# Performance work log

Hardware: AMD Instinct MI355X
Metric: run time of the kernel (lower is better)

## Reference

```python
import jax, jax.numpy as jnp
import numpy as np

B, N, F, S = 32, 512, 101, 10   # batch, set size, str_fea_len, expansion_size
E, H, L = 128, 4, 3             # embed_dim, num_heads, n_encoders
EH = E * H
TAB = 100                       # atom-feature table rows


def _ln(x, g, b, eps=1e-5):
    m = jnp.mean(x, -1, keepdims=True)
    v = jnp.var(x, -1, keepdims=True)
    return (x - m) / jnp.sqrt(v + eps) * g + b


def setup_inputs() -> dict:
    key = jax.random.key(0)
    ks = iter(jax.random.split(key, 48))
    nrm = lambda shape: jax.random.normal(next(ks), shape, jnp.float32) * 0.05
    return {
        'str_fea': jax.random.uniform(next(ks), (B, N, F), jnp.float32),
        'comp_fea': jax.random.randint(next(ks), (B, N), 0, TAB),
        'cell_fea': jax.random.normal(next(ks), (B, 6), jnp.float32),
        'af_table': jax.random.uniform(next(ks), (TAB, 92), jnp.float32),
        'comp_w': nrm((92, E)), 'comp_b': jnp.zeros((E,), jnp.float32),
        'emb_w': nrm(((F - 1) * S, E)), 'emb_b': jnp.zeros((E,), jnp.float32),
        'ln_g': jnp.ones((L, E), jnp.float32), 'ln_b': jnp.zeros((L, E), jnp.float32),
        'wq': nrm((L, E, EH)), 'bq': jnp.zeros((L, EH), jnp.float32),
        'wk': nrm((L, E, EH)), 'bk': jnp.zeros((L, EH), jnp.float32),
        'wv': nrm((L, E, EH)), 'bv': jnp.zeros((L, EH), jnp.float32),
        'inproj_w': nrm((L, EH, 3 * EH)), 'inproj_b': jnp.zeros((L, 3 * EH), jnp.float32),
        'out_w': nrm((L, EH, E)), 'out_b': jnp.zeros((L, E), jnp.float32),
        'ffn_w': nrm((L, E, E)), 'ffn_b': jnp.zeros((L, E), jnp.float32),
        'ln2_g': jnp.ones((E,), jnp.float32), 'ln2_b': jnp.zeros((E,), jnp.float32),
        'final_w': nrm((E, 1)), 'final_b': jnp.zeros((1,), jnp.float32),
    }


def reference(str_fea, comp_fea, cell_fea, af_table, comp_w, comp_b, emb_w, emb_b,
              ln_g, ln_b, wq, bq, wk, bk, wv, bv, inproj_w, inproj_b,
              out_w, out_b, ffn_w, ffn_b, ln2_g, ln2_b, final_w, final_b):
    weights = str_fea[:, :, 0:1]                                  # [B,N,1]
    # AtomFeaturizer + composition embedding
    comp = af_table[comp_fea] @ comp_w + comp_b                   # [B,N,E]
    # DistanceExpansion: (1 - (d - i/S))**2 for i in 0..S-1
    d = str_fea[:, :, 1:]                                         # [B,N,F-1]
    starter = jnp.arange(S, dtype=str_fea.dtype) / S
    de = (1.0 - (d[..., None] - starter)) ** 2                    # [B,N,F-1,S]
    de = de.reshape(d.shape[0], d.shape[1], (F - 1) * S)
    strf = de @ emb_w + emb_b                                     # [B,N,E]
    x = comp + strf
    x_init = x
    mask = jnp.sum(weights, -1) == 0.0                            # [B,N] key padding
    w_row = weights[..., 0]                                       # [B,N]
    hd = EH // H
    scale = 1.0 / np.sqrt(hd)
    for l in range(L):
        xn = _ln(x, ln_g[l], ln_b[l])
        qin = xn @ wq[l] + bq[l]                                  # [B,N,EH]
        kin = xn @ wk[l] + bk[l]
        vin = xn @ wv[l] + bv[l]                                  # used as V in manual attention
        # torch.nn.MultiheadAttention in-projection (v-block unused: att_output discarded)
        q = qin @ inproj_w[l][:, :EH] + inproj_b[l][:EH]
        k = kin @ inproj_w[l][:, EH:2 * EH] + inproj_b[l][EH:2 * EH]
        qh = q.reshape(q.shape[0], q.shape[1], H, hd)
        kh = k.reshape(k.shape[0], k.shape[1], H, hd)
        logits = jnp.einsum('bihd,bjhd->bhij', qh, kh) * scale    # [B,H,N,N]
        logits = jnp.where(mask[:, None, None, :], -1e9, logits)
        attn = jnp.mean(jax.nn.softmax(logits, -1), axis=1)       # head-averaged [B,N,N]
        # external edge-weight masking + renormalization
        aw = attn * w_row[:, None, :]
        aw = aw / jnp.sum(aw, -1, keepdims=True)
        att_out = jnp.einsum('bij,bjd->bid', aw, vin)             # [B,N,EH]
        o1 = x + att_out @ out_w[l] + out_b[l]
        o2 = jax.nn.softplus(_ln(o1, ln_g[l], ln_b[l]) @ ffn_w[l] + ffn_b[l])
        x = _ln(o1 + o2, ln_g[l], ln_b[l])
    x = jnp.sum(weights * (x + x_init), axis=1)                   # weighted pool [B,E]
    x = _ln(x, ln2_g, ln2_b)
    return x @ final_w + final_b                                  # [B,1]
```

## Files before the change

kernel.cpp:

```cpp
#include <hip/hip_runtime.h>
#include <math.h>

#define B_ 32
#define N_ 512
#define F_ 101
#define E_ 128
#define H_ 4
#define EH_ 512
#define L_ 3
#define M_ (B_*N_)

typedef __attribute__((ext_vector_type(8))) short s8v;
typedef __attribute__((ext_vector_type(8))) unsigned short us8v;
typedef __attribute__((ext_vector_type(4))) float f4v;
typedef __attribute__((ext_vector_type(4))) unsigned int u4v;

__device__ __forceinline__ unsigned short f2bf(float f){
  unsigned int u = __builtin_bit_cast(unsigned int, f);
  u += 0x7fffu + ((u>>16)&1u);
  return (unsigned short)(u>>16);
}
__device__ __forceinline__ float bf2f(unsigned int h){
  unsigned int u = h<<16; return __builtin_bit_cast(float, u);
}
__device__ __forceinline__ float softplus_f(float v) {
  return fmaxf(v, 0.f) + log1pf(__expf(-fabsf(v)));
}

#define GLOAD16(gp, lp) __builtin_amdgcn_global_load_lds( \
    (__attribute__((address_space(1))) unsigned int*)(gp), \
    (__attribute__((address_space(3))) unsigned int*)(lp), 16, 0, 0)

#define MFMA16(a,b,c) __builtin_amdgcn_mfma_f32_16x16x32_bf16(a,b,c,0,0,0)

__global__ __launch_bounds__(256) void prepA_kernel(
    const float* __restrict__ wq, const float* __restrict__ wk,
    const float* __restrict__ bq, const float* __restrict__ bk,
    const float* __restrict__ inproj_w,
    float* __restrict__ effpart, float* __restrict__ bpart) {
  __shared__ float As[64][132];
  __shared__ float Bs[64][68];
  const int blk = blockIdx.x;
  const int t = threadIdx.x;
  if (blk < 384) {
    const int bx = blk % 48, ks = blk / 48;
    const int lq = bx>>3, nt = bx&7;
    const int l = lq>>1, qk = lq&1;
    const int bn = nt*64;
    const int k0 = ks*64;
    const float* A = (qk ? wk : wq) + (size_t)l*128*512;
    const float* IP = inproj_w + (size_t)l*512*1536 + qk*512 + bn;
    float acc[8][4];
    #pragma unroll
    for (int i=0;i<8;++i)
      #pragma unroll
      for (int j=0;j<4;++j) acc[i][j]=0.f;
    const int r0 = (t&15)*8, c0 = (t>>4)*4;
    {
      int r = t & 127, half = t>>7;
      #pragma unroll
      for (int u=0;u<8;++u){
        float4 a = *(const float4*)(A + (size_t)r*512 + k0 + half*32 + u*4);
        int kk = half*32 + u*4;
        As[kk+0][r]=a.x; As[kk+1][r]=a.y; As[kk+2][r]=a.z; As[kk+3][r]=a.w;
      }
      int kk = t>>2, cb = (t&3)*16;
      #pragma unroll
      for (int u=0;u<4;++u)
        *(float4*)&Bs[kk][cb+u*4] = *(const float4*)(IP + (size_t)(k0+kk)*1536 + cb + u*4);
    }
    __syncthreads();
    for (int k2=0;k2<64;++k2){
      float4 b = *(const float4*)&Bs[k2][c0];
      float4 a0 = *(const float4*)&As[k2][r0];
      float4 a1 = *(const float4*)&As[k2][r0+4];
      float av[8] = {a0.x,a0.y,a0.z,a0.w,a1.x,a1.y,a1.z,a1.w};
      #pragma unroll
      for (int i=0;i<8;++i){
        acc[i][0] += av[i]*b.x; acc[i][1] += av[i]*b.y;
        acc[i][2] += av[i]*b.z; acc[i][3] += av[i]*b.w;
      }
    }
    #pragma unroll
    for (int j=0;j<4;++j){
      float* dst = effpart + (((size_t)ks*48 + bx)*64 + c0 + j)*128 + r0;
      float4 v0 = {acc[0][j], acc[1][j], acc[2][j], acc[3][j]};
      float4 v1 = {acc[4][j], acc[5][j], acc[6][j], acc[7][j]};
      *(float4*)dst = v0;
      *(float4*)(dst+4) = v1;
    }
  } else {
    const int idxb = blk - 384;
    const int lq = idxb>>3, kt = idxb&7;
    const int l = lq>>1, qk = lq&1;
    const float* bv = (qk?bk:bq) + l*512 + kt*64;
    const float* IP = inproj_w + ((size_t)l*512 + kt*64)*1536 + qk*512;
    float a0=0.f, a1=0.f;
    for (int kk=0; kk<64; ++kk){
      float b = bv[kk];
      const float* row = IP + (size_t)kk*1536;
      a0 += b*row[t];
      a1 += b*row[t+256];
    }
    bpart[(lq*8+kt)*512 + t]       = a0;
    bpart[(lq*8+kt)*512 + t + 256] = a1;
  }
}

__global__ __launch_bounds__(256) void prepB_kernel(
    const float* __restrict__ effpart, const float* __restrict__ bpart,
    const float* __restrict__ wv, const float* __restrict__ out_w,
    const float* __restrict__ ffn_w,
    const float* __restrict__ inproj_b, const float* __restrict__ bvv,
    const float* __restrict__ emb_w, const float* __restrict__ comp_w,
    const float* __restrict__ str_fea, const int* __restrict__ comp_fea,
    const float* __restrict__ af_table,
    unsigned short* __restrict__ wqkvT, unsigned short* __restrict__ outT,
    unsigned short* __restrict__ ffnT, float* __restrict__ bqkv,
    unsigned short* __restrict__ WHi, unsigned short* __restrict__ WLo,
    float* __restrict__ Cpart,
    unsigned short* __restrict__ FHi, unsigned short* __restrict__ FLo,
    float* __restrict__ w_row) {
  const int blk = blockIdx.x;
  const int t = threadIdx.x;
  if (blk < 1536) {
    int idx = blk*256 + t;
    int m = idx & 127;
    int n = (idx>>7) & 511;
    int lq = idx >> 16;
    int l = lq>>1, qk = lq&1;
    size_t base = (((size_t)(lq*8 + (n>>6)))*64 + (n&63))*128 + m;
    float v = 0.f;
    #pragma unroll
    for (int ks=0;ks<8;++ks) v += effpart[(size_t)ks*393216 + base];
    wqkvT[((size_t)l*1536 + qk*512 + n)*128 + m] = f2bf(v);
  } else if (blk < 1662) {
    const int b2 = blk - 1536;
    if (b2 < 108) {
      __shared__ float tile[64][65];
      const float* src; unsigned short* dst; int srcld, dstld;
      if (b2 < 48) {
        int lay = b2/16, rem = b2%16, kt = rem>>3, nt = rem&7;
        src = wv + ((size_t)lay*128 + kt*64)*512 + nt*64; srcld = 512;
        dst = wqkvT + ((size_t)lay*1536 + 1024 + nt*64)*128 + kt*64; dstld = 128;
      } else if (b2 < 96) {
        int b3 = b2-48; int lay = b3/16, rem = b3%16, kt = rem>>1, nt = rem&1;
        src = out_w + ((size_t)lay*512 + kt*64)*128 + nt*64; srcld = 128;
        dst = outT + ((size_t)lay*128 + nt*64)*512 + kt*64; dstld = 512;
      } else {
        int b4 = b2-96; int lay = b4/4, rem = b4%4, kt = rem>>1, nt = rem&1;
        src = ffn_w + ((size_t)lay*128 + kt*64)*128 + nt*64; srcld = 128;
        dst = ffnT + ((size_t)lay*128 + nt*64)*128 + kt*64; dstld = 128;
      }
      #pragma unroll
      for (int rp=0; rp<4; ++rp){
        int r = rp*16 + (t>>4), c = (t&15)*4;
        float4 v = *(const float4*)(src + (size_t)r*srcld + c);
        tile[r][c+0]=v.x; tile[r][c+1]=v.y; tile[r][c+2]=v.z; tile[r][c+3]=v.w;
      }
      __syncthreads();
      #pragma unroll
      for (int wp=0; wp<2; ++wp){
        int n = wp*32 + (t>>3), kk = (t&7)*8;
        us8v pk;
        #pragma unroll
        for (int e=0;e<8;++e) pk[e] = f2bf(tile[kk+e][n]);
        *(us8v*)(dst + (size_t)n*dstld + kk) = pk;
      }
    } else {
      int idx = (b2-108)*256 + t;
      if (idx < 4608) {
        int l = idx/1536, n = idx - l*1536;
        float v;
        if (n < 1024) {
          int qk = n>>9, c = n&511;
          v = inproj_b[(size_t)l*1536 + n];
          #pragma unroll
          for (int kt=0;kt<8;++kt) v += bpart[((l*2+qk)*8+kt)*512 + c];
        } else {
          v = bvv[(size_t)l*512 + (n-1024)];
        }
        bqkv[idx] = v;
      }
    }
  } else if (blk < 1674) {
    if (t < 128) {
      int p = blk - 1662, e = t;
      if (p < 10) {
        float Cp = 0.f;
        for (int ff=0; ff<10; ++ff){
          int f = p*10+ff;
          float A=0.f, Bv=0.f;
          #pragma unroll
          for (int s=0;s<10;++s){
            float wvv = emb_w[(size_t)(f*10+s)*128 + e];
            A += wvv; Bv += 0.2f*s*wvv; Cp += 0.01f*(s*s)*wvv;
          }
          int kA = 92+f, kB = 192+f;
          unsigned short hA = f2bf(A);
          WHi[e*320+kA]=hA; WLo[e*320+kA]=f2bf(A - bf2f(hA));
          unsigned short hB = f2bf(Bv);
          WHi[e*320+kB]=hB; WLo[e*320+kB]=f2bf(Bv - bf2f(hB));
        }
        Cpart[p*128+e] = Cp;
      } else if (p == 10) {
        for (int kk=0;kk<92;++kk){
          float v = comp_w[(size_t)kk*128 + e];
          unsigned short h = f2bf(v);
          WHi[e*320+kk]=h; WLo[e*320+kk]=f2bf(v - bf2f(h));
        }
      } else {
        for (int kk=292;kk<320;++kk){ WHi[e*320+kk]=0; WLo[e*320+kk]=0; }
      }
    }
  } else {
    int g = (blk-1674)*256 + t;
    int row = g / 40, seg = g - row*40;
    const float* sr = str_fea + (size_t)row*F_;
    if (seg == 0) w_row[row] = sr[0];
    const float* af = af_table + (size_t)comp_fea[row]*92;
    const int c0 = seg*8;
    us8v hi, lo;
    #pragma unroll
    for (int e=0;e<8;++e){
      int kk = c0+e; float v;
      if (kk < 92) v = af[kk];
      else if (kk < 192) { float u = 1.f - sr[1+kk-92]; v = u*u; }
      else if (kk < 292) v = 1.f - sr[1+kk-192];
      else v = 0.f;
      unsigned short h = f2bf(v);
      hi[e] = h; lo[e] = f2bf(v - bf2f(h));
    }
    *(us8v*)(FHi + (size_t)row*320 + c0) = hi;
    *(us8v*)(FLo + (size_t)row*320 + c0) = lo;
  }
}

__global__ __launch_bounds__(256) void embgemm_kernel(
    const unsigned short* __restrict__ FHi, const unsigned short* __restrict__ FLo,
    const unsigned short* __restrict__ WHi, const unsigned short* __restrict__ WLo,
    const float* __restrict__ Cpart, const float* __restrict__ comp_b,
    const float* __restrict__ emb_b,
    const float* __restrict__ g0, const float* __restrict__ b0,
    float* __restrict__ x, float* __restrict__ x_init,
    unsigned short* __restrict__ xnb) {
  __shared__ unsigned short lds[24576];
  unsigned short* AHi = lds;
  unsigned short* ALo = lds + 4096;
  unsigned short* BHi = lds + 8192;
  unsigned short* BLo = lds + 16384;
  const int bm = blockIdx.x*64;
  const int t = threadIdx.x, w = t>>6, l = t&63;
  f4v acc[8];
  #pragma unroll
  for (int i=0;i<8;++i) acc[i] = (f4v){0.f,0.f,0.f,0.f};
  const int srow = t>>3, sseg = t&7;
  for (int k0=0;k0<320;k0+=64){
    #pragma unroll
    for (int c=0;c<2;++c){
      int row = c*32+srow;
      GLOAD16(FHi + (size_t)(bm+row)*320 + k0 + ((sseg^(row&7))<<3), (char*)AHi + c*4096 + w*1024);
      GLOAD16(FLo + (size_t)(bm+row)*320 + k0 + ((sseg^(row&7))<<3), (char*)ALo + c*4096 + w*1024);
    }
    #pragma unroll
    for (int c=0;c<4;++c){
      int row = c*32+srow;
      GLOAD16(WHi + (size_t)row*320 + k0 + ((sseg^(row&7))<<3), (char*)BHi + c*4096 + w*1024);
      GLOAD16(WLo + (size_t)row*320 + k0 + ((sseg^(row&7))<<3), (char*)BLo + c*4096 + w*1024);
    }
    __syncthreads();
    #pragma unroll
    for (int ks=0;ks<2;++ks){
      int arow = w*16 + (l&15);
      int aswz = ((((l>>4)+ks*4) ^ (arow&7))<<4);
      s8v ah = *(const s8v*)((const char*)AHi + arow*128 + aswz);
      s8v al = *(const s8v*)((const char*)ALo + arow*128 + aswz);
      #pragma unroll
      for (int ct=0;ct<8;++ct){
        int col = ct*16 + (l&15);
        int bswz = ((((l>>4)+ks*4) ^ (col&7))<<4);
        s8v bh = *(const s8v*)((const char*)BHi + col*128 + bswz);
        s8v bl = *(const s8v*)((const char*)BLo + col*128 + bswz);
        acc[ct] = MFMA16(ah, bh, acc[ct]);
        acc[ct] = MFMA16(ah, bl, acc[ct]);
        acc[ct] = MFMA16(al, bh, acc[ct]);
      }
    }
    __syncthreads();
  }
  float vv[8][4], gc[8], bc[8];
  #pragma unroll
  for (int ct=0;ct<8;++ct){
    int c = ct*16 + (l&15);
    float be = comp_b[c] + emb_b[c];
    for (int p=0;p<10;++p) be += Cpart[p*128+c];
    gc[ct] = g0[c]; bc[ct] = b0[c];
    #pragma unroll
    for (int r=0;r<4;++r) vv[ct][r] = acc[ct][r] + be;
  }
  #pragma unroll
  for (int r=0;r<4;++r){
    float s=0.f, sq=0.f;
    #pragma unroll
    for (int ct=0;ct<8;++ct){ s += vv[ct][r]; sq += vv[ct][r]*vv[ct][r]; }
    #pragma unroll
    for (int m=1;m<16;m<<=1){ s += __shfl_xor(s,m,64); sq += __shfl_xor(sq,m,64); }
    float mean = s*(1.f/128.f);
    float rstd = rsqrtf(sq*(1.f/128.f) - mean*mean + 1e-5f);
    int row = bm + w*16 + (l>>4)*4 + r;
    #pragma unroll
    for (int ct=0;ct<8;++ct){
      int c = ct*16 + (l&15);
      float v = vv[ct][r];
      x[(size_t)row*128 + c] = v;
      x_init[(size_t)row*128 + c] = v;
      xnb[(size_t)row*128 + c] = f2bf((v-mean)*rstd*gc[ct] + bc[ct]);
    }
  }
}

template<int RT>
__global__ __launch_bounds__(256) void mgemm_kernel(
    const unsigned short* __restrict__ A,
    const unsigned short* __restrict__ Bt,
    const float* __restrict__ bias,
    unsigned short* __restrict__ Cb,
    unsigned short* __restrict__ vT,
    int K) {
  constexpr int BM = RT*32;
  __shared__ float smem[8192];
  unsigned short* Al = (unsigned short*)smem;
  unsigned short* Bl = Al + BM*64;
  const int bm = blockIdx.x*BM;
  const int bn = blockIdx.y*128;
  const int t = threadIdx.x;
  const int w = t>>6, l = t&63;
  const int wr = w>>1, wc = w&1;
  f4v acc[RT][4];
  #pragma unroll
  for (int i=0;i<RT;++i)
    #pragma unroll
    for (int j=0;j<4;++j) acc[i][j] = (f4v){0.f,0.f,0.f,0.f};
  const int srow = t>>3, sseg = t&7;
  for (int k0 = 0; k0 < K; k0 += 64) {
    #pragma unroll
    for (int c=0;c<BM/32;++c){
      int row = c*32 + srow;
      GLOAD16(A + (size_t)(bm+row)*K + k0 + ((sseg ^ (row&7))<<3),
              (char*)Al + c*4096 + w*1024);
    }
    #pragma unroll
    for (int c=0;c<4;++c){
      int row = c*32 + srow;
      GLOAD16(Bt + (size_t)(bn+row)*K + k0 + ((sseg ^ (row&7))<<3),
              (char*)Bl + c*4096 + w*1024);
    }
    __syncthreads();
    #pragma unroll
    for (int ks=0;ks<2;++ks){
      s8v bf[4];
      #pragma unroll
      for (int ct=0;ct<4;++ct){
        int col = wc*64 + ct*16 + (l&15);
        bf[ct] = *(const s8v*)((const char*)Bl + col*128 + ((((l>>4)+ks*4) ^ (col&7))<<4));
      }
      #pragma unroll
      for (int rt=0;rt<RT;++rt){
        int arow = wr*(RT*16) + rt*16 + (l&15);
        s8v af = *(const s8v*)((const char*)Al + arow*128 + ((((l>>4)+ks*4) ^ (arow&7))<<4));
        #pragma unroll
        for (int ct=0;ct<4;++ct)
          acc[rt][ct] = MFMA16(af, bf[ct], acc[rt][ct]);
      }
    }
    __syncthreads();
  }
  float bia[4];
  #pragma unroll
  for (int ct=0;ct<4;++ct) bia[ct] = bias[bn + wc*64 + ct*16 + (l&15)];
  unsigned short* lds16 = (unsigned short*)smem;
  if (bn < 1024) {
    #pragma unroll
    for (int rt=0;rt<RT;++rt)
      #pragma unroll
      for (int ct=0;ct<4;++ct)
        #pragma unroll
        for (int r=0;r<4;++r){
          int rr = wr*(RT*16) + rt*16 + (l>>4)*4 + r;
          int cc = wc*64 + ct*16 + (l&15);
          lds16[rr*128 + cc] = f2bf(acc[rt][ct][r] + bia[ct]);
        }
    __syncthreads();
    #pragma unroll
    for (int it=0; it<BM/16; ++it){
      int row = it*16 + (t>>4), seg = t&15;
      u4v v = *(const u4v*)(lds16 + row*128 + seg*8);
      *(u4v*)(Cb + (size_t)(bm+row)*1024 + bn + seg*8) = v;
    }
  } else {
    #pragma unroll
    for (int rt=0;rt<RT;++rt)
      #pragma unroll
      for (int ct=0;ct<4;++ct){
        int rbase = bm + wr*(RT*16) + rt*16 + (l>>4)*4;
        int bb = rbase >> 9, nn = rbase & 511;
        int d = bn - 1024 + wc*64 + ct*16 + (l&15);
        unsigned int lo = (unsigned int)f2bf(acc[rt][ct][0] + bia[ct])
                        | ((unsigned int)f2bf(acc[rt][ct][1] + bia[ct])<<16);
        unsigned int hi = (unsigned int)f2bf(acc[rt][ct][2] + bia[ct])
                        | ((unsigned int)f2bf(acc[rt][ct][3] + bia[ct])<<16);
        uint2 pk; pk.x = lo; pk.y = hi;
        *(uint2*)(vT + ((size_t)(bb*512 + d))*512 + nn) = pk;
      }
  }
}

#define STG_K5(dst, j0s) { \
  _Pragma("unroll") \
  for (int c_=0;c_<8;++c_){ \
    int row_ = c_*8 + w; \
    GLOAD16(qkb + (size_t)(b*512 + (j0s) + row_)*1024 + 512 + ((l ^ (row_&7))<<3), \
            (dst) + row_*1024); } }

#define STG_V5(j0s) { \
  _Pragma("unroll") \
  for (int c_=0;c_<8;++c_){ \
    int dbase_ = (c_*8 + w)*8; \
    GLOAD16(vT + ((size_t)(b*512 + dbase_ + (l>>3)))*512 + (j0s) + (((l&7) ^ (l>>3))<<3), \
            Vl + dbase_*128); } }

#define STG_B1(dst, k0s) { \
  _Pragma("unroll") \
  for (int c_=0;c_<2;++c_){ \
    int n_ = c_*64 + w*8 + (l>>3); \
    GLOAD16(outTl + (size_t)n_*512 + (k0s) + (((l&7) ^ (n_&7))<<3), \
            (dst) + (c_*64 + w*8)*128); } }

#define STG_F1() { \
  _Pragma("unroll") \
  for (int c2_=0;c2_<4;++c2_){ \
    int kh_ = c2_>>1, c_ = c2_&1; \
    int n_ = c_*64 + w*8 + (l>>3); \
    GLOAD16(ffnTl + (size_t)n_*128 + kh_*64 + (((l&7) ^ (n_&7))<<3), \
            ffnB + kh_*16384 + (c_*64 + w*8)*128); } }

__global__ __launch_bounds__(512, 2) void attnT_kernel(
    const unsigned short* __restrict__ qkb, const unsigned short* __restrict__ vT,
    const float* __restrict__ w_row,
    const unsigned short* __restrict__ outTl, const float* __restrict__ out_b,
    const unsigned short* __restrict__ ffnTl, const float* __restrict__ ffn_b,
    float* __restrict__ x, unsigned short* __restrict__ xnb,
    const float* __restrict__ g1, const float* __restrict__ b1,
    const float* __restrict__ g2, const float* __restrict__ b2) {
  __shared__ char smem[148736];
  char* const KbA = smem;
  char* const KbB = smem + 65536;
  char* const cA  = smem + 131072;
  float* const w_s    = (float*)(smem + 140288);
  float* const Spart  = (float*)(smem + 142336);
  float* const Rpart  = (float*)(smem + 144384);
  float* const sinv_l = (float*)(smem + 146432);
  float* const rho_l  = (float*)(smem + 147456);
  float* const zinv_l = (float*)(smem + 148480);
  char* const Vl = KbB;
  unsigned short* const outL = (unsigned short*)smem;
  char* const BtA = smem + 81920;
  char* const BtB = smem + 98304;
  float* const vst = (float*)(smem + 114688);
  char* const xnl  = smem;
  char* const ffnB = smem + 16384;

  const int id = blockIdx.x;
  const int b  = (id & 7) | ((id >> 6) << 3);
  const int i0 = ((id >> 3) & 7) * 64;
  const int bm = b*512 + i0;
  const int t = threadIdx.x, w = t>>6, l = t&63;
  const int wi = w & 3, wd = w >> 2;
  const float SC2 = 1.4426950408889634f * 0.088388347648318447f;

  for (int j=t; j<512; j+=512) w_s[j] = w_row[b*512+j];

  s8v qf[4][4];
  {
    const unsigned short* qbase = qkb + ((size_t)(b*512 + i0 + wi*16 + (l&15)))*1024;
    #pragma unroll
    for (int h=0;h<4;++h)
      #pragma unroll
      for (int ks=0;ks<4;++ks)
        qf[h][ks] = *(const s8v*)(qbase + h*128 + ks*32 + (l>>4)*8);
  }

  float sp[4][4], rp[4][4];
  #pragma unroll
  for (int h=0;h<4;++h)
    #pragma unroll
    for (int r=0;r<4;++r){ sp[h][r]=0.f; rp[h][r]=0.f; }

  STG_K5(KbA, 0);
  __syncthreads();

  {
    char* Kc = KbA; char* Kn = KbB;
    #pragma unroll 1
    for (int tt=0; tt<8; ++tt){
      if (tt < 7) STG_K5(Kn, (tt+1)*64);
      #pragma unroll
      for (int jsub=0;jsub<2;++jsub){
        const int jcol = wd*32 + jsub*16 + (l&15);
        const float wv = w_s[tt*64 + jcol];
        const float mw = (wv != 0.f) ? 1.f : 0.f;
        #pragma unroll
        for (int h=0;h<4;++h){
          f4v a = (f4v){0.f,0.f,0.f,0.f};
          #pragma unroll
          for (int ks=0;ks<4;++ks){
            int g = h*16 + ks*4 + (l>>4);
            s8v kf = *(const s8v*)(Kc + jcol*1024 + ((g ^ (jcol&7))<<4));
            a = MFMA16(qf[h][ks], kf, a);
          }
          #pragma unroll
          for (int r=0;r<4;++r){
            float e = exp2f(a[r]*SC2);
            sp[h][r] += e*mw;
            rp[h][r] += e*wv;
          }
        }
      }
      __syncthreads();
      char* tmp = Kc; Kc = Kn; Kn = tmp;
    }
  }

  #pragma unroll
  for (int h=0;h<4;++h)
    #pragma unroll
    for (int r=0;r<4;++r){
      float s = sp[h][r], rv = rp[h][r];
      s += __shfl_xor(s,1,64); rv += __shfl_xor(rv,1,64);
      s += __shfl_xor(s,2,64); rv += __shfl_xor(rv,2,64);
      s += __shfl_xor(s,4,64); rv += __shfl_xor(rv,4,64);
      s += __shfl_xor(s,8,64); rv += __shfl_xor(rv,8,64);
      sp[h][r] = s; rp[h][r] = rv;
    }
  if ((l&15)==0){
    int i = wi*16 + (l>>4)*4;
    #pragma unroll
    for (int h=0;h<4;++h)
      #pragma unroll
      for (int r=0;r<4;++r){
        Spart[(wd*4+h)*64 + i + r] = sp[h][r];
        Rpart[(wd*4+h)*64 + i + r] = rp[h][r];
      }
  }
  STG_K5(KbA, 0);
  STG_V5(0);
  __syncthreads();
  if (t < 256){
    int h = t>>6, i = t&63;
    float S = Spart[h*64+i] + Spart[(4+h)*64+i];
    float R = Rpart[h*64+i] + Rpart[(4+h)*64+i];
    float si = 1.f/S;
    sinv_l[h*64+i] = si;
    rho_l[h*64+i]  = R*si;
  }
  __syncthreads();
  if (t < 64)
    zinv_l[t] = 1.f/(rho_l[t] + rho_l[64+t] + rho_l[128+t] + rho_l[192+t]);
  __syncthreads();

  float siv[4][4], zv[4];
  {
    int ib = wi*16 + (l>>4)*4;
    #pragma unroll
    for (int h=0;h<4;++h)
      #pragma unroll
      for (int r=0;r<4;++r) siv[h][r] = sinv_l[h*64 + ib + r];
    #pragma unroll
    for (int r=0;r<4;++r) zv[r] = zinv_l[ib + r];
  }

  char* const Kl = KbA;
  f4v pacc[16];
  #pragma unroll
  for (int ct=0;ct<16;++ct) pacc[ct] = (f4v){0.f,0.f,0.f,0.f};
  const int arow = wi*16 + (l&15);
  #pragma unroll 1
  for (int tt=0; tt<8; ++tt){
    float cacc[2][4];
    #pragma unroll
    for (int jsub=0;jsub<2;++jsub){
      const int jcol = wd*32 + jsub*16 + (l&15);
      #pragma unroll
      for (int r=0;r<4;++r) cacc[jsub][r] = 0.f;
      #pragma unroll
      for (int h=0;h<4;++h){
        f4v a = (f4v){0.f,0.f,0.f,0.f};
        #pragma unroll
        for (int ks=0;ks<4;++ks){
          int g = h*16 + ks*4 + (l>>4);
          s8v kf = *(const s8v*)(Kl + jcol*1024 + ((g ^ (jcol&7))<<4));
          a = MFMA16(qf[h][ks], kf, a);
        }
        #pragma unroll
        for (int r=0;r<4;++r)
          cacc[jsub][r] += exp2f(a[r]*SC2) * siv[h][r];
      }
      float wv2 = w_s[tt*64 + jcol];
      #pragma unroll
      for (int r=0;r<4;++r){
        int i = wi*16 + (l>>4)*4 + r;
        *(unsigned short*)(cA + i*144 + jcol*2) = f2bf(cacc[jsub][r]*wv2);
      }
    }
    __syncthreads();
    if (tt < 7) STG_K5(Kl, (tt+1)*64);
    #pragma unroll
    for (int ks=0;ks<2;++ks){
      int kidx = (l>>4) + ks*4;
      s8v af = *(const s8v*)(cA + arow*144 + (kidx<<4));
      #pragma unroll
      for (int ct=0;ct<16;++ct){
        int d = wd*256 + ct*16 + (l&15);
        s8v vf = *(const s8v*)(Vl + d*128 + ((kidx ^ (d&7))<<4));
        pacc[ct] = MFMA16(af, vf, pacc[ct]);
      }
    }
    __syncthreads();
    if (tt < 7) STG_V5((tt+1)*64);
  }

  #pragma unroll
  for (int ct=0;ct<16;++ct){
    int d = wd*256 + ct*16 + (l&15);
    #pragma unroll
    for (int r=0;r<4;++r){
      int i = wi*16 + (l>>4)*4 + r;
      outL[i*520 + d] = f2bf(pacc[ct][r]*zv[r]);
    }
  }
  STG_B1(BtA, 0);
  __syncthreads();

  f4v acc1[4];
  #pragma unroll
  for (int ct=0;ct<4;++ct) acc1[ct] = (f4v){0.f,0.f,0.f,0.f};
  {
    char* Bc = BtA; char* Bn = BtB;
    #pragma unroll 1
    for (int tt=0; tt<8; ++tt){
      if (tt < 7) STG_B1(Bn, (tt+1)*64);
      #pragma unroll
      for (int ks=0;ks<2;++ks){
        int kidx = (l>>4) + ks*4;
        s8v af = *(const s8v*)((const char*)outL + arow*1040 + tt*128 + (kidx<<4));
        #pragma unroll
        for (int ct=0;ct<4;++ct){
          int n = wd*64 + ct*16 + (l&15);
          s8v bf = *(const s8v*)(Bc + n*128 + ((kidx ^ (n&7))<<4));
          acc1[ct] = MFMA16(af, bf, acc1[ct]);
        }
      }
      __syncthreads();
      char* tmp = Bc; Bc = Bn; Bn = tmp;
    }
  }

  #pragma unroll
  for (int ct=0;ct<4;++ct){
    int cc = wd*64 + ct*16 + (l&15);
    float ob = out_b[cc];
    #pragma unroll
    for (int r=0;r<4;++r){
      int rr = wi*16 + (l>>4)*4 + r;
      vst[rr*128 + cc] = acc1[ct][r] + ob + x[(size_t)(bm+rr)*128 + cc];
    }
  }
  STG_F1();
  __syncthreads();

  {
    const float2 g1v = *(const float2*)(g1 + l*2);
    const float2 b1v = *(const float2*)(b1 + l*2);
    #pragma unroll
    for (int rr=0; rr<8; ++rr){
      int row = w*8 + rr;
      float2 vv = *(const float2*)&vst[row*128 + l*2];
      float s = vv.x+vv.y, sq = vv.x*vv.x + vv.y*vv.y;
      #pragma unroll
      for (int m=1;m<64;m<<=1){ s += __shfl_xor(s,m,64); sq += __shfl_xor(sq,m,64); }
      float mean = s*(1.f/128.f);
      float rstd = rsqrtf(sq*(1.f/128.f) - mean*mean + 1e-5f);
      float xa = (vv.x-mean)*rstd*g1v.x + b1v.x;
      float xb = (vv.y-mean)*rstd*g1v.y + b1v.y;
      int col = l*2;
      int byte = row*256 + (((col>>3) ^ (row&7))<<4) + ((col&7)<<1);
      unsigned int pk = (unsigned int)f2bf(xa) | ((unsigned int)f2bf(xb)<<16);
      *(unsigned int*)(xnl + byte) = pk;
    }
  }
  __syncthreads();

  f4v acc2[4];
  #pragma unroll
  for (int ct=0;ct<4;++ct) acc2[ct] = (f4v){0.f,0.f,0.f,0.f};
  #pragma unroll
  for (int ks2=0;ks2<4;++ks2){
    int kidx2 = (l>>4) + ks2*4;
    s8v af = *(const s8v*)(xnl + arow*256 + ((kidx2 ^ (arow&7))<<4));
    int kh = ks2>>1, ksb = ks2&1;
    int kb = (l>>4) + ksb*4;
    #pragma unroll
    for (int ct=0;ct<4;++ct){
      int n = wd*64 + ct*16 + (l&15);
      s8v bf = *(const s8v*)(ffnB + kh*16384 + n*128 + ((kb ^ (n&7))<<4));
      acc2[ct] = MFMA16(af, bf, acc2[ct]);
    }
  }
  #pragma unroll
  for (int ct=0;ct<4;++ct){
    int cc = wd*64 + ct*16 + (l&15);
    float fb = ffn_b[cc];
    #pragma unroll
    for (int r=0;r<4;++r){
      int rr = wi*16 + (l>>4)*4 + r;
      vst[rr*128 + cc] += softplus_f(acc2[ct][r] + fb);
    }
  }
  __syncthreads();

  {
    const float2 g1v = *(const float2*)(g1 + l*2);
    const float2 b1v = *(const float2*)(b1 + l*2);
    #pragma unroll
    for (int rr=0; rr<8; ++rr){
      int row = w*8 + rr;
      float2 vv = *(const float2*)&vst[row*128 + l*2];
      float s = vv.x+vv.y, sq = vv.x*vv.x + vv.y*vv.y;
      #pragma unroll
      for (int m=1;m<64;m<<=1){ s += __shfl_xor(s,m,64); sq += __shfl_xor(sq,m,64); }
      float mean = s*(1.f/128.f);
      float rstd = rsqrtf(sq*(1.f/128.f) - mean*mean + 1e-5f);
      float xa = (vv.x-mean)*rstd*g1v.x + b1v.x;
      float xb = (vv.y-mean)*rstd*g1v.y + b1v.y;
      float2 xo; xo.x = xa; xo.y = xb;
      *(float2*)(x + (size_t)(bm+row)*128 + l*2) = xo;
      if (g2) {
        float s2 = xa+xb, sq2 = xa*xa + xb*xb;
        #pragma unroll
        for (int m=1;m<64;m<<=1){ s2 += __shfl_xor(s2,m,64); sq2 += __shfl_xor(sq2,m,64); }
        float mean2 = s2*(1.f/128.f);
        float rstd2 = rsqrtf(sq2*(1.f/128.f) - mean2*mean2 + 1e-5f);
        const float2 g2v = *(const float2*)(g2 + l*2);
        const float2 b2v = *(const float2*)(b2 + l*2);
        float ya = (xa-mean2)*rstd2*g2v.x + b2v.x;
        float yb = (xb-mean2)*rstd2*g2v.y + b2v.y;
        unsigned int pk = (unsigned int)f2bf(ya) | ((unsigned int)f2bf(yb)<<16);
        *(unsigned int*)(xnb + (size_t)(bm+row)*128 + l*2) = pk;
      }
    }
  }
}

__global__ __launch_bounds__(256) void poolfinal_kernel(
    const float* __restrict__ x, const float* __restrict__ x_init,
    const float* __restrict__ w_row,
    const float* __restrict__ g, const float* __restrict__ bt,
    const float* __restrict__ fw, const float* __restrict__ fb,
    float* __restrict__ out) {
  __shared__ float red[2][128];
  __shared__ float red2[4];
  __shared__ float red3[2];
  const int b = blockIdx.x;
  const int t = threadIdx.x;
  const int e = t & 127, half = t >> 7;
  float acc = 0.f;
  for (int n = half*256; n < half*256+256; ++n) {
    float w = w_row[(size_t)b*N_ + n];
    size_t o = ((size_t)b*N_ + n)*E_ + e;
    acc += w * (x[o] + x_init[o]);
  }
  red[half][e] = acc;
  __syncthreads();
  float s=0.f, sq=0.f, v=0.f;
  if (t < 128) {
    v = red[0][t] + red[1][t];
    s = v; sq = v*v;
    #pragma unroll
    for (int m = 1; m < 64; m <<= 1) { s += __shfl_xor(s, m, 64); sq += __shfl_xor(sq, m, 64); }
    if ((t&63) == 0) { red2[(t>>6)*2] = s; red2[(t>>6)*2+1] = sq; }
  }
  __syncthreads();
  float p = 0.f;
  if (t < 128) {
    s = red2[0] + red2[2]; sq = red2[1] + red2[3];
    float mean = s*(1.f/E_), var = sq*(1.f/E_) - mean*mean;
    float rstd = rsqrtf(var + 1e-5f);
    float xl = (v - mean)*rstd*g[t] + bt[t];
    p = xl * fw[t];
    #pragma unroll
    for (int m = 1; m < 64; m <<= 1) p += __shfl_xor(p, m, 64);
    if ((t&63) == 0) red3[t>>6] = p;
  }
  __syncthreads();
  if (t == 0) out[b] = red3[0] + red3[1] + fb[0];
}

extern "C" void kernel_launch(void* const* d_in, const int* in_sizes, int n_in,
                              void* d_out, int out_size, void* d_ws, size_t ws_size,
                              hipStream_t stream) {
  (void)in_sizes; (void)n_in; (void)out_size; (void)ws_size;
  const float* str_fea  = (const float*)d_in[0];
  const int*   comp_fea = (const int*)  d_in[1];
  const float* af_table = (const float*)d_in[3];
  const float* comp_w   = (const float*)d_in[4];
  const float* comp_b   = (const float*)d_in[5];
  const float* emb_w    = (const float*)d_in[6];
  const float* emb_b    = (const float*)d_in[7];
  const float* ln_g     = (const float*)d_in[8];
  const float* ln_b     = (const float*)d_in[9];
  const float* wq       = (const float*)d_in[10];
  const float* bq       = (const float*)d_in[11];
  const float* wk       = (const float*)d_in[12];
  const float* bk       = (const float*)d_in[13];
  const float* wv       = (const float*)d_in[14];
  const float* bv       = (const float*)d_in[15];
  const float* inproj_w = (const float*)d_in[16];
  const float* inproj_b = (const float*)d_in[17];
  const float* out_w    = (const float*)d_in[18];
  const float* out_b    = (const float*)d_in[19];
  const float* ffn_w    = (const float*)d_in[20];
  const float* ffn_b    = (const float*)d_in[21];
  const float* ln2_g    = (const float*)d_in[22];
  const float* ln2_b    = (const float*)d_in[23];
  const float* final_w  = (const float*)d_in[24];
  const float* final_b  = (const float*)d_in[25];
  float* out = (float*)d_out;

  float* ws = (float*)d_ws;
  size_t off = 0;
  float* x      = ws + off; off += 2097152;
  float* x_init = ws + off; off += 2097152;
  float* w_row  = ws + off; off += 16384;
  unsigned short* xnb  = (unsigned short*)(ws + off); off += 1048576;
  unsigned short* qkb  = (unsigned short*)(ws + off); off += 8388608;
  unsigned short* vTb  = (unsigned short*)(ws + off); off += 4194304;
  float* bpart  = ws + off; off += 24576;
  float* effpart= ws + off; off += 3145728;
  float* bqkv   = ws + off; off += 4608;
  unsigned short* wqkvT = (unsigned short*)(ws + off); off += 294912;
  unsigned short* outT  = (unsigned short*)(ws + off); off += 98304;
  unsigned short* ffnT  = (unsigned short*)(ws + off); off += 24576;
  unsigned short* FHi   = (unsigned short*)(ws + off); off += 2621440;
  unsigned short* FLo   = (unsigned short*)(ws + off); off += 2621440;
  unsigned short* WHi   = (unsigned short*)(ws + off); off += 20480;
  unsigned short* WLo   = (unsigned short*)(ws + off); off += 20480;
  float* Cpart  = ws + off; off += 1280;

  prepA_kernel<<<432, 256, 0, stream>>>(wq, wk, bq, bk, inproj_w, effpart, bpart);
  prepB_kernel<<<4234, 256, 0, stream>>>(effpart, bpart, wv, out_w, ffn_w,
                                         inproj_b, bv, emb_w, comp_w,
                                         str_fea, comp_fea, af_table,
                                         wqkvT, outT, ffnT, bqkv,
                                         WHi, WLo, Cpart, FHi, FLo, w_row);
  embgemm_kernel<<<M_/64, 256, 0, stream>>>(FHi, FLo, WHi, WLo, Cpart, comp_b, emb_b,
                                            ln_g, ln_b, x, x_init, xnb);

  for (int l = 0; l < L_; ++l) {
    mgemm_kernel<4><<<dim3(M_/128, 12), 256, 0, stream>>>(
        xnb, wqkvT + (size_t)l*196608, bqkv + l*1536, qkb, vTb, 128);
    attnT_kernel<<<256, 512, 0, stream>>>(
        qkb, vTb, w_row,
        outT + (size_t)l*65536, out_b + (size_t)l*E_,
        ffnT + (size_t)l*16384, ffn_b + (size_t)l*E_,
        x, xnb, ln_g + l*E_, ln_b + l*E_,
        (l < 2) ? (ln_g + (l+1)*E_) : nullptr,
        (l < 2) ? (ln_b + (l+1)*E_) : nullptr);
  }

  poolfinal_kernel<<<B_, 256, 0, stream>>>(x, x_init, w_row, ln2_g, ln2_b,
                                           final_w, final_b, out);
}
```

Measured before the change: 349.3 us.

## Compute attention logits once per head and keep exponentials in registers

The attention kernel used to compute the QK^T logits twice, once to get softmax denominators and once to form the head-averaged weights. It now loops head by head, loading a per-head K slice, and keeps every exponential for all 512 keys in registers. It reduces the row sums and then accumulates the normalized combined weights directly. The combined weight matrix is written to LDS once, and the PV GEMM then streams V tiles through a smaller double buffer. This halves the QK MFMA and exp work but raises register pressure and adds syncs per head.

```diff
diff --git a/kernel.cpp b/kernel.cpp
--- a/kernel.cpp
+++ b/kernel.cpp
@@ -415,19 +415,19 @@
   }
 }
 
-#define STG_K5(dst, j0s) { \
+#define STG_KH(dst, hh, j0s) { \
   _Pragma("unroll") \
   for (int c_=0;c_<8;++c_){ \
-    int row_ = c_*8 + w; \
-    GLOAD16(qkb + (size_t)(b*512 + (j0s) + row_)*1024 + 512 + ((l ^ (row_&7))<<3), \
-            (dst) + row_*1024); } }
-
-#define STG_V5(j0s) { \
+    int row_ = c_*32 + w*4 + (l>>4); \
+    GLOAD16(qkb + (size_t)(b*512 + (j0s) + row_)*1024 + 512 + (hh)*128 + (((l&15) ^ (row_&7))<<3), \
+            (dst) + c_*8192 + w*1024); } }
+
+#define STG_VT(dst, j0s) { \
   _Pragma("unroll") \
-  for (int c_=0;c_<8;++c_){ \
-    int dbase_ = (c_*8 + w)*8; \
-    GLOAD16(vT + ((size_t)(b*512 + dbase_ + (l>>3)))*512 + (j0s) + (((l&7) ^ (l>>3))<<3), \
-            Vl + dbase_*128); } }
+  for (int c_=0;c_<4;++c_){ \
+    int d_ = c_*128 + w*16 + (l>>2); \
+    GLOAD16(vT + ((size_t)(b*512 + d_))*512 + (j0s) + (((l&3) ^ ((d_>>1)&3))<<3), \
+            (dst) + c_*8192 + w*1024); } }
 
 #define STG_B1(dst, k0s) { \
   _Pragma("unroll") \
@@ -444,7 +444,7 @@
     GLOAD16(ffnTl + (size_t)n_*128 + kh_*64 + (((l&7) ^ (n_&7))<<3), \
             ffnB + kh_*16384 + (c_*64 + w*8)*128); } }
 
-__global__ __launch_bounds__(512, 2) void attnT_kernel(
+__global__ __launch_bounds__(512, 2) void attnU_kernel(
     const unsigned short* __restrict__ qkb, const unsigned short* __restrict__ vT,
     const float* __restrict__ w_row,
     const unsigned short* __restrict__ outTl, const float* __restrict__ out_b,
@@ -452,21 +452,23 @@
     float* __restrict__ x, unsigned short* __restrict__ xnb,
     const float* __restrict__ g1, const float* __restrict__ b1,
     const float* __restrict__ g2, const float* __restrict__ b2) {
-  __shared__ char smem[148736];
-  char* const KbA = smem;
-  char* const KbB = smem + 65536;
-  char* const cA  = smem + 131072;
-  float* const w_s    = (float*)(smem + 140288);
-  float* const Spart  = (float*)(smem + 142336);
-  float* const Rpart  = (float*)(smem + 144384);
-  float* const sinv_l = (float*)(smem + 146432);
-  float* const rho_l  = (float*)(smem + 147456);
-  float* const zinv_l = (float*)(smem + 148480);
-  char* const Vl = KbB;
+  __shared__ char smem[136704];
+  char* const Kt0 = smem;
+  char* const Kt1 = smem + 65536;
+  char* const cALc = smem;
+  unsigned short* const cAL = (unsigned short*)smem;
+  char* const VbA = smem + 66560;
+  char* const VbB = smem + 99328;
+  float* const w_s    = (float*)(smem + 132096);
+  float* const Spart  = (float*)(smem + 134144);
+  float* const Rpart  = (float*)(smem + 134656);
+  float* const sinv_l = (float*)(smem + 135168);
+  float* const rho_l  = (float*)(smem + 135424);
+  float* const zinv_l = (float*)(smem + 136448);
   unsigned short* const outL = (unsigned short*)smem;
-  char* const BtA = smem + 81920;
-  char* const BtB = smem + 98304;
-  float* const vst = (float*)(smem + 114688);
+  char* const BtA = smem + 66560;
+  char* const BtB = smem + 82944;
+  float* const vst = (float*)(smem + 99328);
   char* const xnl  = smem;
   char* const ffnB = smem + 16384;
 
@@ -476,167 +478,150 @@
   const int bm = b*512 + i0;
   const int t = threadIdx.x, w = t>>6, l = t&63;
   const int wi = w & 3, wd = w >> 2;
+  const int ib = wi*16 + (l>>4)*4;
+  const int arow = wi*16 + (l&15);
   const float SC2 = 1.4426950408889634f * 0.088388347648318447f;
 
   for (int j=t; j<512; j+=512) w_s[j] = w_row[b*512+j];
 
-  s8v qf[4][4];
-  {
-    const unsigned short* qbase = qkb + ((size_t)(b*512 + i0 + wi*16 + (l&15)))*1024;
-    #pragma unroll
-    for (int h=0;h<4;++h)
-      #pragma unroll
-      for (int ks=0;ks<4;++ks)
-        qf[h][ks] = *(const s8v*)(qbase + h*128 + ks*32 + (l>>4)*8);
-  }
-
-  float sp[4][4], rp[4][4];
-  #pragma unroll
-  for (int h=0;h<4;++h)
-    #pragma unroll
-    for (int r=0;r<4;++r){ sp[h][r]=0.f; rp[h][r]=0.f; }
-
-  STG_K5(KbA, 0);
+  float c_[2][8][4];
+  #pragma unroll
+  for (int tt=0;tt<2;++tt)
+    #pragma unroll
+    for (int js=0;js<8;++js)
+      #pragma unroll
+      for (int r=0;r<4;++r) c_[tt][js][r] = 0.f;
+
+  STG_KH(Kt0, 0, 0);
   __syncthreads();
 
-  {
-    char* Kc = KbA; char* Kn = KbB;
-    #pragma unroll 1
-    for (int tt=0; tt<8; ++tt){
-      if (tt < 7) STG_K5(Kn, (tt+1)*64);
-      #pragma unroll
-      for (int jsub=0;jsub<2;++jsub){
-        const int jcol = wd*32 + jsub*16 + (l&15);
-        const float wv = w_s[tt*64 + jcol];
-        const float mw = (wv != 0.f) ? 1.f : 0.f;
+  char* Kc = Kt0; char* Kn = Kt1;
+  #pragma unroll 1
+  for (int h=0; h<4; ++h){
+    s8v qf[4];
+    {
+      const unsigned short* qbase = qkb + ((size_t)(bm + arow))*1024 + h*128;
+      #pragma unroll
+      for (int ks=0;ks<4;++ks) qf[ks] = *(const s8v*)(qbase + ks*32 + (l>>4)*8);
+    }
+    float Ex[2][8][4];
+    #pragma unroll
+    for (int tt=0; tt<2; ++tt){
+      if (tt==0) { STG_KH(Kn, h, 256); }
+      else if (h<3) { STG_KH(Kn, h+1, 0); }
+      #pragma unroll
+      for (int jsub=0;jsub<8;++jsub){
+        const int jcol = wd*128 + jsub*16 + (l&15);
+        f4v a = (f4v){0.f,0.f,0.f,0.f};
         #pragma unroll
-        for (int h=0;h<4;++h){
-          f4v a = (f4v){0.f,0.f,0.f,0.f};
-          #pragma unroll
-          for (int ks=0;ks<4;++ks){
-            int g = h*16 + ks*4 + (l>>4);
-            s8v kf = *(const s8v*)(Kc + jcol*1024 + ((g ^ (jcol&7))<<4));
-            a = MFMA16(qf[h][ks], kf, a);
-          }
-          #pragma unroll
-          for (int r=0;r<4;++r){
-            float e = exp2f(a[r]*SC2);
-            sp[h][r] += e*mw;
-            rp[h][r] += e*wv;
-          }
+        for (int ks=0;ks<4;++ks){
+          int g = ks*4 + (l>>4);
+          s8v kf = *(const s8v*)(Kc + jcol*256 + ((g ^ (jcol&7))<<4));
+          a = MFMA16(qf[ks], kf, a);
         }
+        #pragma unroll
+        for (int r=0;r<4;++r) Ex[tt][jsub][r] = exp2f(a[r]*SC2);
       }
       __syncthreads();
       char* tmp = Kc; Kc = Kn; Kn = tmp;
     }
-  }
-
-  #pragma unroll
-  for (int h=0;h<4;++h)
+    float sp[4] = {0.f,0.f,0.f,0.f};
+    float rp[4] = {0.f,0.f,0.f,0.f};
+    #pragma unroll
+    for (int tt=0;tt<2;++tt)
+      #pragma unroll
+      for (int jsub=0;jsub<8;++jsub){
+        int jg = tt*256 + wd*128 + jsub*16 + (l&15);
+        float wv = w_s[jg];
+        float mw = (wv != 0.f) ? 1.f : 0.f;
+        #pragma unroll
+        for (int r=0;r<4;++r){
+          sp[r] += Ex[tt][jsub][r]*mw;
+          rp[r] += Ex[tt][jsub][r]*wv;
+        }
+      }
     #pragma unroll
     for (int r=0;r<4;++r){
-      float s = sp[h][r], rv = rp[h][r];
+      float s = sp[r], rv = rp[r];
       s += __shfl_xor(s,1,64); rv += __shfl_xor(rv,1,64);
       s += __shfl_xor(s,2,64); rv += __shfl_xor(rv,2,64);
       s += __shfl_xor(s,4,64); rv += __shfl_xor(rv,4,64);
       s += __shfl_xor(s,8,64); rv += __shfl_xor(rv,8,64);
-      sp[h][r] = s; rp[h][r] = rv;
-    }
-  if ((l&15)==0){
-    int i = wi*16 + (l>>4)*4;
-    #pragma unroll
-    for (int h=0;h<4;++h)
+      sp[r] = s; rp[r] = rv;
+    }
+    if ((l&15)==0){
       #pragma unroll
       for (int r=0;r<4;++r){
-        Spart[(wd*4+h)*64 + i + r] = sp[h][r];
-        Rpart[(wd*4+h)*64 + i + r] = rp[h][r];
-      }
-  }
-  STG_K5(KbA, 0);
-  STG_V5(0);
-  __syncthreads();
-  if (t < 256){
-    int h = t>>6, i = t&63;
-    float S = Spart[h*64+i] + Spart[(4+h)*64+i];
-    float R = Rpart[h*64+i] + Rpart[(4+h)*64+i];
-    float si = 1.f/S;
-    sinv_l[h*64+i] = si;
-    rho_l[h*64+i]  = R*si;
-  }
-  __syncthreads();
+        Spart[wd*64 + ib + r] = sp[r];
+        Rpart[wd*64 + ib + r] = rp[r];
+      }
+    }
+    __syncthreads();
+    if (t < 64){
+      float S = Spart[t] + Spart[64+t];
+      float R = Rpart[t] + Rpart[64+t];
+      float si = 1.f/S;
+      sinv_l[t] = si;
+      rho_l[h*64+t] = R*si;
+    }
+    __syncthreads();
+    float siv[4];
+    #pragma unroll
+    for (int r=0;r<4;++r) siv[r] = sinv_l[ib + r];
+    #pragma unroll
+    for (int tt=0;tt<2;++tt)
+      #pragma unroll
+      for (int jsub=0;jsub<8;++jsub)
+        #pragma unroll
+        for (int r=0;r<4;++r)
+          c_[tt][jsub][r] += Ex[tt][jsub][r]*siv[r];
+  }
+
+  STG_VT(VbA, 0);
   if (t < 64)
     zinv_l[t] = 1.f/(rho_l[t] + rho_l[64+t] + rho_l[128+t] + rho_l[192+t]);
+  #pragma unroll
+  for (int tt=0;tt<2;++tt)
+    #pragma unroll
+    for (int jsub=0;jsub<8;++jsub){
+      int jg = tt*256 + wd*128 + jsub*16 + (l&15);
+      float wv = w_s[jg];
+      #pragma unroll
+      for (int r=0;r<4;++r)
+        cAL[(ib+r)*520 + jg] = f2bf(c_[tt][jsub][r]*wv);
+    }
   __syncthreads();
-
-  float siv[4][4], zv[4];
+  float zv[4];
+  #pragma unroll
+  for (int r=0;r<4;++r) zv[r] = zinv_l[ib + r];
+
+  f4v pacc[16];
+  #pragma unroll
+  for (int ct=0;ct<16;++ct) pacc[ct] = (f4v){0.f,0.f,0.f,0.f};
   {
-    int ib = wi*16 + (l>>4)*4;
-    #pragma unroll
-    for (int h=0;h<4;++h)
-      #pragma unroll
-      for (int r=0;r<4;++r) siv[h][r] = sinv_l[h*64 + ib + r];
-    #pragma unroll
-    for (int r=0;r<4;++r) zv[r] = zinv_l[ib + r];
-  }
-
-  char* const Kl = KbA;
-  f4v pacc[16];
-  #pragma unroll
-  for (int ct=0;ct<16;++ct) pacc[ct] = (f4v){0.f,0.f,0.f,0.f};
-  const int arow = wi*16 + (l&15);
-  #pragma unroll 1
-  for (int tt=0; tt<8; ++tt){
-    float cacc[2][4];
-    #pragma unroll
-    for (int jsub=0;jsub<2;++jsub){
-      const int jcol = wd*32 + jsub*16 + (l&15);
-      #pragma unroll
-      for (int r=0;r<4;++r) cacc[jsub][r] = 0.f;
-      #pragma unroll
-      for (int h=0;h<4;++h){
-        f4v a = (f4v){0.f,0.f,0.f,0.f};
-        #pragma unroll
-        for (int ks=0;ks<4;++ks){
-          int g = h*16 + ks*4 + (l>>4);
-          s8v kf = *(const s8v*)(Kl + jcol*1024 + ((g ^ (jcol&7))<<4));
-          a = MFMA16(qf[h][ks], kf, a);
-        }
-        #pragma unroll
-        for (int r=0;r<4;++r)
-          cacc[jsub][r] += exp2f(a[r]*SC2) * siv[h][r];
-      }
-      float wv2 = w_s[tt*64 + jcol];
-      #pragma unroll
-      for (int r=0;r<4;++r){
-        int i = wi*16 + (l>>4)*4 + r;
-        *(unsigned short*)(cA + i*144 + jcol*2) = f2bf(cacc[jsub][r]*wv2);
-      }
-    }
-    __syncthreads();
-    if (tt < 7) STG_K5(Kl, (tt+1)*64);
-    #pragma unroll
-    for (int ks=0;ks<2;++ks){
-      int kidx = (l>>4) + ks*4;
-      s8v af = *(const s8v*)(cA + arow*144 + (kidx<<4));
+    char* Vc = VbA; char* Vn = VbB;
+    #pragma unroll 1
+    for (int vt=0; vt<16; ++vt){
+      if (vt < 15) STG_VT(Vn, (vt+1)*32);
+      int kidx = l>>4;
+      s8v af = *(const s8v*)(cALc + arow*1040 + vt*64 + (kidx<<4));
       #pragma unroll
       for (int ct=0;ct<16;++ct){
         int d = wd*256 + ct*16 + (l&15);
-        s8v vf = *(const s8v*)(Vl + d*128 + ((kidx ^ (d&7))<<4));
+        s8v vf = *(const s8v*)(Vc + d*64 + ((kidx ^ ((d>>1)&3))<<4));
         pacc[ct] = MFMA16(af, vf, pacc[ct]);
       }
-    }
-    __syncthreads();
-    if (tt < 7) STG_V5((tt+1)*64);
+      __syncthreads();
+      char* tmp = Vc; Vc = Vn; Vn = tmp;
+    }
   }
 
   #pragma unroll
   for (int ct=0;ct<16;++ct){
     int d = wd*256 + ct*16 + (l&15);
     #pragma unroll
-    for (int r=0;r<4;++r){
-      int i = wi*16 + (l>>4)*4 + r;
-      outL[i*520 + d] = f2bf(pacc[ct][r]*zv[r]);
-    }
+    for (int r=0;r<4;++r)
+      outL[(ib+r)*520 + d] = f2bf(pacc[ct][r]*zv[r]);
   }
   STG_B1(BtA, 0);
   __syncthreads();
@@ -868,7 +853,7 @@
   for (int l = 0; l < L_; ++l) {
     mgemm_kernel<4><<<dim3(M_/128, 12), 256, 0, stream>>>(
         xnb, wqkvT + (size_t)l*196608, bqkv + l*1536, qkb, vTb, 128);
-    attnT_kernel<<<256, 512, 0, stream>>>(
+    attnU_kernel<<<256, 512, 0, stream>>>(
         qkb, vTb, w_row,
         outT + (size_t)l*65536, out_b + (size_t)l*E_,
         ffnT + (size_t)l*16384, ffn_b + (size_t)l*E_,
```

New measurement: 304.3 us. 12.9% less time.
